# Kernel optimization log

Hardware: AMD Instinct MI355X
Metric: run time of the kernel (lower is better)

Reference implementation:

```python
import jax, jax.numpy as jnp
import numpy as np

CENTER = 7          # center_size
K = 5               # neighbourhood_size
DIL = 1             # dilation
EPS_LN = 1e-5       # torch F.layer_norm default eps
EPS_COS = 1e-8      # torch F.cosine_similarity default eps


def _unfold_image(image, k):
    """torch F.unfold(image, k, stride=1, padding=k//2) -> [B, T, C*k*k]."""
    B, C, H, W = image.shape
    p = k // 2
    padded = jnp.pad(image, ((0, 0), (0, 0), (p, p), (p, p)))
    # channel-major patch layout (c, ki, kj), matching torch.unfold
    patches = jnp.stack([padded[:, :, i:i + H, j:j + W]
                         for i in range(k) for j in range(k)], axis=2)  # [B,C,k*k,H,W]
    return patches.reshape(B, C * k * k, H * W).transpose(0, 2, 1)       # [B,T,D]


def _neighbour_indices(H, W, k, dil):
    """generate_local_indices with constant padding value N=H*W, center removed -> [T, k*k-1]."""
    half = (k - 1) // 2 * dil
    N = H * W
    inds = np.arange(N).reshape(H, W)
    padded = np.full((H + 2 * half, W + 2 * half), N, dtype=np.int64)
    padded[half:half + H, half:half + W] = inds
    cols = [padded[i * dil:i * dil + H, j * dil:j * dil + W].reshape(-1)
            for i in range(k) for j in range(k)]
    local = np.stack(cols, axis=-1)  # [T, k*k]
    center = (k * k) // 2
    keep = [s for s in range(k * k) if s != center]
    return jnp.asarray(local[:, keep])  # [T, S], S = k*k-1


def setup_inputs() -> dict:
    key = jax.random.key(0)
    image = jax.random.uniform(key, (2, 3, 128, 128), dtype=jnp.float32)
    return {"image": image}


def reference(image):
    B, C, H, W = image.shape
    T = H * W
    kc = CENTER

    # im2col of center patches: [B, T, C*kc*kc]
    bu = _unfold_image(image, kc)

    # per-channel LayerNorm over kc*kc elements (no affine), then +1.0 twice
    bu = bu.reshape(B, T, C, kc * kc)
    mu = bu.mean(axis=-1, keepdims=True)
    var = ((bu - mu) ** 2).mean(axis=-1, keepdims=True)
    bu = (bu - mu) / jnp.sqrt(var + EPS_LN)
    bu = bu.reshape(B, T, C * kc * kc) + 2.0  # [B,T,D]

    # local neighbourhood indices (padding index == T marks out-of-bounds)
    nb = _neighbour_indices(H, W, K, DIL)  # [T, S]

    # gather surround patches; row T is the invalid (zero) row
    bu_ext = jnp.concatenate([bu, jnp.zeros((B, 1, bu.shape[-1]), bu.dtype)], axis=1)
    surround = bu_ext[:, nb]  # [B,T,S,D]

    # cosine similarity between each center patch and its S neighbours
    dot = jnp.einsum('btd,btsd->bts', bu, surround)
    n_node = jnp.linalg.norm(bu, axis=-1)        # [B,T]
    n_sur = jnp.linalg.norm(surround, axis=-1)   # [B,T,S]
    cos = dot / jnp.maximum(n_node[:, :, None] * n_sur, EPS_COS)
    dist = (1.0 - cos) * 0.5  # = 1 - (1+cos)/2

    # masked mean over valid neighbours
    mask = (nb != T).astype(dist.dtype)  # [T,S]
    sal = (dist * mask).sum(-1) / mask.sum(-1)
    return sal.reshape(B, H, W)
```

## Files before the change

kernel.cpp:

```cpp
#include <hip/hip_runtime.h>

#define HH 128
#define WW 128
#define CC 3
#define TX 16
#define TY 8
#define NPIX (TX*TY)
#define SW (TX+4)
#define SH (TY+4)
#define NST (SW*SH)
#define IW (TX+10)
#define IH (TY+10)
#define NIMG (IW*IH)
#define PSTRIDE 25
#define NTHR 384

__global__ __launch_bounds__(NTHR, 1)
void err_neurons_kernel(const float* __restrict__ img, float* __restrict__ out) {
    __shared__ float s_img[CC][NIMG];
    __shared__ float s_mu[CC][NST];
    __shared__ float s_r[CC][NST];
    __shared__ float s_nsqc[CC][NST];
    __shared__ float s_nrm[NST];
    __shared__ float s_part[CC][NPIX * PSTRIDE];

    const int tid = threadIdx.x;
    const int bx = blockIdx.x, by = blockIdx.y, b = blockIdx.z;
    const int x0 = bx * TX, y0 = by * TY;
    const float* imgb = img + (size_t)b * CC * HH * WW;

    for (int i = tid; i < CC * NIMG; i += NTHR) {
        int c = i / NIMG, r = i % NIMG;
        int iy = r / IW, ix = r % IW;
        int yy = y0 - 5 + iy, xx = x0 - 5 + ix;
        float v = 0.f;
        if (yy >= 0 && yy < HH && xx >= 0 && xx < WW)
            v = imgb[(size_t)c * HH * WW + yy * WW + xx];
        s_img[c][r] = v;
    }
    __syncthreads();

    for (int s = tid; s < CC * NST; s += NTHR) {
        int c = s / NST, pos = s % NST;
        int sy = pos / SW, sx = pos % SW;
        const float* base = &s_img[c][sy * IW + sx];
        float sum = 0.f, sum2 = 0.f;
#pragma unroll
        for (int i = 0; i < 7; ++i)
#pragma unroll
            for (int j = 0; j < 7; ++j) {
                float v = base[i * IW + j];
                sum += v; sum2 = fmaf(v, v, sum2);
            }
        float mu  = sum * (1.f / 49.f);
        float var = fmaf(-mu, mu, sum2 * (1.f / 49.f));
        var = fmaxf(var, 0.f);
        float r = rsqrtf(var + 1e-5f);
        s_mu[c][pos] = mu;
        s_r[c][pos]  = r;
        s_nsqc[c][pos] = fmaf(49.f * var, r * r, 196.f);
    }
    __syncthreads();
    if (tid < NST)
        s_nrm[tid] = sqrtf(s_nsqc[0][tid] + s_nsqc[1][tid] + s_nsqc[2][tid]);
    __syncthreads();

    {
        const int p = tid % NPIX, c = tid / NPIX;
        const int x = p % TX, y = p / TX;
        float R[11][11];
#pragma unroll
        for (int a = 0; a < 11; ++a)
#pragma unroll
            for (int bb = 0; bb < 11; ++bb)
                R[a][bb] = s_img[c][(y + a) * IW + (x + bb)];
        const int cpos = (y + 2) * SW + (x + 2);
        const float mut = s_mu[c][cpos];
        const float rt  = s_r[c][cpos];
#pragma unroll
        for (int u = 0; u < 25; ++u) {
            if (u == 12) continue;
            const int dy = u / 5 - 2, dx = u % 5 - 2;
            const int j = u - (u > 12 ? 1 : 0);
            float cross = 0.f;
#pragma unroll
            for (int oy = 0; oy < 7; ++oy)
#pragma unroll
                for (int ox = 0; ox < 7; ++ox)
                    cross = fmaf(R[oy + 2][ox + 2], R[oy + 2 + dy][ox + 2 + dx], cross);
            const int upos = (y + 2 + dy) * SW + (x + 2 + dx);
            float part = (cross - 49.f * mut * s_mu[c][upos]) * rt * s_r[c][upos];
            s_part[c][p * PSTRIDE + j] = part;
        }
    }
    __syncthreads();

    if (tid < NPIX) {
        const int p = tid;
        const int x = p % TX, y = p / TX;
        const int gx = x0 + x, gy = y0 + y;
        const float nt = s_nrm[(y + 2) * SW + (x + 2)];
        float acc = 0.f, cnt = 0.f;
#pragma unroll
        for (int u = 0; u < 25; ++u) {
            if (u == 12) continue;
            const int dy = u / 5 - 2, dx = u % 5 - 2;
            const int j = u - (u > 12 ? 1 : 0);
            if (gy + dy < 0 || gy + dy >= HH || gx + dx < 0 || gx + dx >= WW) continue;
            float dot = 588.f + s_part[0][p * PSTRIDE + j]
                              + s_part[1][p * PSTRIDE + j]
                              + s_part[2][p * PSTRIDE + j];
            const float nu = s_nrm[(y + 2 + dy) * SW + (x + 2 + dx)];
            float cosv = dot / fmaxf(nt * nu, 1e-8f);
            acc += (1.f - cosv) * 0.5f;
            cnt += 1.f;
        }
        out[(size_t)b * HH * WW + gy * WW + gx] = acc / cnt;
    }
}

extern "C" void kernel_launch(void* const* d_in, const int* in_sizes, int n_in,
                              void* d_out, int out_size, void* d_ws, size_t ws_size,
                              hipStream_t stream) {
    const float* img = (const float*)d_in[0];
    float* out = (float*)d_out;
    dim3 grid(WW / TX, HH / TY, 2);
    dim3 block(NTHR);
    hipLaunchKernelGGL(err_neurons_kernel, grid, block, 0, stream, img, out);
}
```

Before: 15.43 us.

## Shrink tile to 8x8, split neighbour offsets across thread halves, separable stats

Tiles shrink from 16x8 to 8x8, which doubles the block count, and launch bounds are raised so more blocks fit on each CU. Each pixel-channel's 24 neighbour cross-products are split between two thread groups, each holding a smaller 9x11 register window, which cuts per-thread register pressure and serial work. The 7x7 window sums become separable row sums followed by column sums, and the final cosine uses precomputed reciprocal norms instead of a per-neighbour divide. The cost is a larger relative halo overhead per tile, one extra shared-memory pass and sync, and dropping the 1e-8 clamp on the norm product.

```diff
diff --git a/kernel.cpp b/kernel.cpp
--- a/kernel.cpp
+++ b/kernel.cpp
@@ -3,119 +3,138 @@
 #define HH 128
 #define WW 128
 #define CC 3
-#define TX 16
+#define TX 8
 #define TY 8
-#define NPIX (TX*TY)
-#define SW (TX+4)
-#define SH (TY+4)
-#define NST (SW*SH)
-#define IW (TX+10)
-#define IH (TY+10)
-#define NIMG (IW*IH)
+#define NPIX 64
+#define IW 18
+#define NIMG (IW*IW)
+#define SW 12
+#define NST (SW*SW)
 #define PSTRIDE 25
 #define NTHR 384
 
-__global__ __launch_bounds__(NTHR, 1)
+__global__ __launch_bounds__(NTHR, 3)
 void err_neurons_kernel(const float* __restrict__ img, float* __restrict__ out) {
     __shared__ float s_img[CC][NIMG];
+    __shared__ float s_rs[CC][IW][SW];
+    __shared__ float s_rs2[CC][IW][SW];
     __shared__ float s_mu[CC][NST];
     __shared__ float s_r[CC][NST];
-    __shared__ float s_nsqc[CC][NST];
-    __shared__ float s_nrm[NST];
+    __shared__ float s_nsq[CC][NST];
+    __shared__ float s_rnrm[NST];
     __shared__ float s_part[CC][NPIX * PSTRIDE];
 
     const int tid = threadIdx.x;
-    const int bx = blockIdx.x, by = blockIdx.y, b = blockIdx.z;
-    const int x0 = bx * TX, y0 = by * TY;
-    const float* imgb = img + (size_t)b * CC * HH * WW;
+    const int x0 = blockIdx.x * TX, y0 = blockIdx.y * TY;
+    const float* imgb = img + (size_t)blockIdx.z * CC * HH * WW;
 
     for (int i = tid; i < CC * NIMG; i += NTHR) {
-        int c = i / NIMG, r = i % NIMG;
-        int iy = r / IW, ix = r % IW;
-        int yy = y0 - 5 + iy, xx = x0 - 5 + ix;
+        const int c = i / NIMG, r = i % NIMG;
+        const int iy = r / IW, ix = r % IW;
+        const int yy = y0 - 5 + iy, xx = x0 - 5 + ix;
         float v = 0.f;
-        if (yy >= 0 && yy < HH && xx >= 0 && xx < WW)
+        if ((unsigned)yy < HH && (unsigned)xx < WW)
             v = imgb[(size_t)c * HH * WW + yy * WW + xx];
         s_img[c][r] = v;
     }
     __syncthreads();
 
-    for (int s = tid; s < CC * NST; s += NTHR) {
-        int c = s / NST, pos = s % NST;
-        int sy = pos / SW, sx = pos % SW;
-        const float* base = &s_img[c][sy * IW + sx];
-        float sum = 0.f, sum2 = 0.f;
+    for (int u2 = tid; u2 < CC * IW * SW; u2 += NTHR) {
+        const int c = u2 / (IW * SW);
+        const int rem = u2 % (IW * SW);
+        const int r = rem / SW, sx = rem % SW;
+        const float* bp = &s_img[c][r * IW + sx];
+        float s = 0.f, s2 = 0.f;
 #pragma unroll
-        for (int i = 0; i < 7; ++i)
+        for (int j = 0; j < 7; ++j) { float v = bp[j]; s += v; s2 = fmaf(v, v, s2); }
+        s_rs[c][r][sx] = s; s_rs2[c][r][sx] = s2;
+    }
+    __syncthreads();
+
+    for (int u2 = tid; u2 < CC * NST; u2 += NTHR) {
+        const int c = u2 / NST;
+        const int pos = u2 % NST;
+        const int sy = pos / SW, sx = pos % SW;
+        float s = 0.f, s2 = 0.f;
 #pragma unroll
-            for (int j = 0; j < 7; ++j) {
-                float v = base[i * IW + j];
-                sum += v; sum2 = fmaf(v, v, sum2);
-            }
-        float mu  = sum * (1.f / 49.f);
-        float var = fmaf(-mu, mu, sum2 * (1.f / 49.f));
-        var = fmaxf(var, 0.f);
-        float r = rsqrtf(var + 1e-5f);
+        for (int i = 0; i < 7; ++i) { s += s_rs[c][sy + i][sx]; s2 += s_rs2[c][sy + i][sx]; }
+        const float mu  = s * (1.f / 49.f);
+        const float var = fmaxf(fmaf(-mu, mu, s2 * (1.f / 49.f)), 0.f);
+        const float rr  = rsqrtf(var + 1e-5f);
         s_mu[c][pos] = mu;
-        s_r[c][pos]  = r;
-        s_nsqc[c][pos] = fmaf(49.f * var, r * r, 196.f);
+        s_r[c][pos]  = rr;
+        s_nsq[c][pos] = fmaf(49.f * var, rr * rr, 196.f);
     }
     __syncthreads();
     if (tid < NST)
-        s_nrm[tid] = sqrtf(s_nsqc[0][tid] + s_nsqc[1][tid] + s_nsqc[2][tid]);
+        s_rnrm[tid] = rsqrtf(s_nsq[0][tid] + s_nsq[1][tid] + s_nsq[2][tid]);
     __syncthreads();
 
     {
-        const int p = tid % NPIX, c = tid / NPIX;
-        const int x = p % TX, y = p / TX;
-        float R[11][11];
+        const int p = tid & 63;
+        const int g = tid >> 6;
+        const int c = g % 3, h = g / 3;
+        const int x = p & 7, y = p >> 3;
+        const int row0 = y + 2 * h;
+        float W[9][11];
 #pragma unroll
-        for (int a = 0; a < 11; ++a)
+        for (int r = 0; r < 9; ++r)
 #pragma unroll
-            for (int bb = 0; bb < 11; ++bb)
-                R[a][bb] = s_img[c][(y + a) * IW + (x + bb)];
-        const int cpos = (y + 2) * SW + (x + 2);
-        const float mut = s_mu[c][cpos];
-        const float rt  = s_r[c][cpos];
+            for (int q = 0; q < 11; ++q)
+                W[r][q] = s_img[c][(row0 + r) * IW + x + q];
+        const int spos = (y + 2) * SW + (x + 2);
+        const float mut = s_mu[c][spos];
+        const float rt  = s_r[c][spos];
+        float* partp = &s_part[c][p * PSTRIDE];
+        if (h == 0) {
+#pragma unroll
+            for (int j = 0; j < 12; ++j) {
+                const int dy = j / 5 - 2, dx = j % 5 - 2;
+                float cross = 0.f;
+#pragma unroll
+                for (int oy = 0; oy < 7; ++oy)
+#pragma unroll
+                    for (int ox = 0; ox < 7; ++ox)
+                        cross = fmaf(W[2 + oy][2 + ox], W[2 + dy + oy][2 + dx + ox], cross);
+                const int upos = (y + 2 + dy) * SW + (x + 2 + dx);
+                partp[j] = fmaf(-49.f * mut, s_mu[c][upos], cross) * (rt * s_r[c][upos]);
+            }
+        } else {
+#pragma unroll
+            for (int j = 0; j < 12; ++j) {
+                const int u = j + 13;
+                const int dy = u / 5 - 2, dx = u % 5 - 2;
+                float cross = 0.f;
+#pragma unroll
+                for (int oy = 0; oy < 7; ++oy)
+#pragma unroll
+                    for (int ox = 0; ox < 7; ++ox)
+                        cross = fmaf(W[oy][2 + ox], W[dy + oy][2 + dx + ox], cross);
+                const int upos = (y + 2 + dy) * SW + (x + 2 + dx);
+                partp[j + 12] = fmaf(-49.f * mut, s_mu[c][upos], cross) * (rt * s_r[c][upos]);
+            }
+        }
+    }
+    __syncthreads();
+
+    if (tid < NPIX) {
+        const int p = tid, x = p & 7, y = p >> 3;
+        const int gx = x0 + x, gy = y0 + y;
+        const float rnt = s_rnrm[(y + 2) * SW + (x + 2)];
+        float csum = 0.f, cnt = 0.f;
 #pragma unroll
         for (int u = 0; u < 25; ++u) {
             if (u == 12) continue;
             const int dy = u / 5 - 2, dx = u % 5 - 2;
             const int j = u - (u > 12 ? 1 : 0);
-            float cross = 0.f;
-#pragma unroll
-            for (int oy = 0; oy < 7; ++oy)
-#pragma unroll
-                for (int ox = 0; ox < 7; ++ox)
-                    cross = fmaf(R[oy + 2][ox + 2], R[oy + 2 + dy][ox + 2 + dx], cross);
-            const int upos = (y + 2 + dy) * SW + (x + 2 + dx);
-            float part = (cross - 49.f * mut * s_mu[c][upos]) * rt * s_r[c][upos];
-            s_part[c][p * PSTRIDE + j] = part;
-        }
-    }
-    __syncthreads();
-
-    if (tid < NPIX) {
-        const int p = tid;
-        const int x = p % TX, y = p / TX;
-        const int gx = x0 + x, gy = y0 + y;
-        const float nt = s_nrm[(y + 2) * SW + (x + 2)];
-        float acc = 0.f, cnt = 0.f;
-#pragma unroll
-        for (int u = 0; u < 25; ++u) {
-            if (u == 12) continue;
-            const int dy = u / 5 - 2, dx = u % 5 - 2;
-            const int j = u - (u > 12 ? 1 : 0);
-            if (gy + dy < 0 || gy + dy >= HH || gx + dx < 0 || gx + dx >= WW) continue;
-            float dot = 588.f + s_part[0][p * PSTRIDE + j]
-                              + s_part[1][p * PSTRIDE + j]
-                              + s_part[2][p * PSTRIDE + j];
-            const float nu = s_nrm[(y + 2 + dy) * SW + (x + 2 + dx)];
-            float cosv = dot / fmaxf(nt * nu, 1e-8f);
-            acc += (1.f - cosv) * 0.5f;
+            if ((unsigned)(gy + dy) >= HH || (unsigned)(gx + dx) >= WW) continue;
+            const float dot = 588.f + s_part[0][p * PSTRIDE + j]
+                                    + s_part[1][p * PSTRIDE + j]
+                                    + s_part[2][p * PSTRIDE + j];
+            csum += dot * rnt * s_rnrm[(y + 2 + dy) * SW + (x + 2 + dx)];
             cnt += 1.f;
         }
-        out[(size_t)b * HH * WW + gy * WW + gx] = acc / cnt;
+        out[(size_t)blockIdx.z * HH * WW + gy * WW + gx] = 0.5f - csum / (2.f * cnt);
     }
 }
 
```

Measured after the change: 21.27 us. 37.8% more time.
